# Kernel tuning notes

Measured on AMD Instinct MI355X. Metric: run time of the kernel, lower is better.

## Reference

```python
import jax, jax.numpy as jnp
import numpy as np

N_BASIS = 128   # n_atom_basis F
N_INT   = 3     # n_interactions
N_RBF   = 20
CUTOFF  = 5.0
MAX_Z   = 100
EPS     = 1e-8
N_ATOMS = 25000
N_EDGES = 200000


def setup_inputs() -> dict:
    key = jax.random.key(0)
    ks = jax.random.split(key, 16)
    F = N_BASIS
    s = 0.02
    z     = jax.random.randint(ks[0], (N_ATOMS,), 1, MAX_Z)
    pos   = jax.random.uniform(ks[1], (N_ATOMS, 3), dtype=jnp.float32) * 2.0  # small box -> inside cutoff
    idx_i = jax.random.randint(ks[2], (N_EDGES,), 0, N_ATOMS)
    idx_j = jax.random.randint(ks[3], (N_EDGES,), 0, N_ATOMS)
    emb   = jax.random.normal(ks[4], (MAX_Z, F), dtype=jnp.float32) * s
    fW    = jax.random.normal(ks[5], (N_RBF, 3 * F * N_INT), dtype=jnp.float32) * s
    fb    = jnp.zeros((3 * F * N_INT,), jnp.float32)
    iW1   = jax.random.normal(ks[6], (N_INT, F, F), dtype=jnp.float32) * s
    ib1   = jnp.zeros((N_INT, F), jnp.float32)
    iW2   = jax.random.normal(ks[7], (N_INT, F, 3 * F), dtype=jnp.float32) * s
    ib2   = jnp.zeros((N_INT, 3 * F), jnp.float32)
    mWmix = jax.random.normal(ks[8], (N_INT, F, 2 * F), dtype=jnp.float32) * s
    mW1   = jax.random.normal(ks[9], (N_INT, 2 * F, F), dtype=jnp.float32) * s
    mb1   = jnp.zeros((N_INT, F), jnp.float32)
    mW2   = jax.random.normal(ks[10], (N_INT, F, 3 * F), dtype=jnp.float32) * s
    mb2   = jnp.zeros((N_INT, 3 * F), jnp.float32)
    return dict(z=z, pos=pos, idx_i=idx_i, idx_j=idx_j, emb=emb, fW=fW, fb=fb,
                iW1=iW1, ib1=ib1, iW2=iW2, ib2=ib2,
                mWmix=mWmix, mW1=mW1, mb1=mb1, mW2=mW2, mb2=mb2)


def reference(z, pos, idx_i, idx_j, emb, fW, fb, iW1, ib1, iW2, ib2,
              mWmix, mW1, mb1, mW2, mb2):
    F = N_BASIS
    n_atoms = z.shape[0]
    # geometry
    r_ij = pos[idx_j] - pos[idx_i]                                  # [E,3]
    r_ij = jnp.where(jnp.abs(r_ij) < 1e-6, 1e-6, r_ij)
    d_ij = jnp.linalg.norm(r_ij, axis=1, keepdims=True)             # [E,1]
    dir_ij = r_ij / d_ij                                            # [E,3]
    # Gaussian radial basis
    offsets = jnp.linspace(0.0, CUTOFF, N_RBF)
    width = offsets[1] - offsets[0]
    coeff = -0.5 / (width * width)
    phi = jnp.exp(coeff * (d_ij[..., None] - offsets) ** 2)         # [E,1,n_rbf]
    # cosine cutoff
    fcut = 0.5 * (jnp.cos(jnp.pi * d_ij / CUTOFF) + 1.0) * (d_ij < CUTOFF)  # [E,1]
    filters = (phi @ fW + fb) * fcut[..., None]                     # [E,1,3F*I]
    filter_list = jnp.split(filters, N_INT, axis=-1)                # each [E,1,3F]
    # initial atom features
    q = emb[z][:, None, :]                                          # [N,1,F]
    mu = jnp.zeros((n_atoms, 3, F), q.dtype)                        # [N,3,F]
    for t in range(N_INT):
        # --- interaction (gather - filter-multiply - scatter-add) ---
        x = jax.nn.silu(q @ iW1[t] + ib1[t]) @ iW2[t] + ib2[t]      # [N,1,3F]
        xj = x[idx_j]                                               # [E,1,3F]
        muj = mu[idx_j]                                             # [E,3,F]
        x = filter_list[t] * xj                                     # [E,1,3F]
        dq, dmuR, dmumu = jnp.split(x, 3, axis=-1)                  # [E,1,F] each
        dq = jax.ops.segment_sum(dq, idx_i, num_segments=n_atoms)   # [N,1,F]
        dmu = dmuR * dir_ij[..., None] + dmumu * muj                # [E,3,F]
        dmu = jax.ops.segment_sum(dmu, idx_i, num_segments=n_atoms) # [N,3,F]
        q = q + dq
        mu = mu + dmu
        # --- mixing (intra-atomic) ---
        mu_mix = mu @ mWmix[t]                                      # [N,3,2F]
        mu_V, mu_W = jnp.split(mu_mix, 2, axis=-1)                  # [N,3,F]
        mu_Vn = jnp.sqrt(jnp.sum(mu_V ** 2, axis=-2, keepdims=True) + EPS)  # [N,1,F]
        ctx = jnp.concatenate([q, mu_Vn], axis=-1)                  # [N,1,2F]
        x = jax.nn.silu(ctx @ mW1[t] + mb1[t]) @ mW2[t] + mb2[t]    # [N,1,3F]
        dq_intra, dmu_intra, dqmu_intra = jnp.split(x, 3, axis=-1)
        dmu_intra = dmu_intra * mu_W                                # [N,3,F]
        dqmu_intra = dqmu_intra * jnp.sum(mu_V * mu_W, axis=1, keepdims=True)
        q = q + dq_intra + dqmu_intra
        mu = mu + dmu_intra
    return q.squeeze(1), mu
```

## Files before the change

### kernel.cpp

```cpp
#include <hip/hip_runtime.h>
#include <hip/hip_bf16.h>

#define F 128
#define F3 384
#define NRBF 20
#define NITER 3
#define KP 24

typedef __hip_bfloat16 bf16;
typedef __bf16 bfrag __attribute__((ext_vector_type(8)));
typedef float f32x4 __attribute__((ext_vector_type(4)));

__device__ __forceinline__ float b2f(bf16 v) { return __bfloat162float(v); }
__device__ __forceinline__ bf16 f2b(float v) { return __float2bfloat16(v); }
__device__ __forceinline__ bfrag ldb(const bf16* p) { return *(const bfrag*)p; }
__device__ __forceinline__ bfrag ldsb(const __bf16* p) { return *(const bfrag*)p; }
__device__ __forceinline__ bfrag cvtf(const float* p) {
    bfrag r;
#pragma unroll
    for (int j = 0; j < 8; ++j) r[j] = (__bf16)p[j];
    return r;
}

__global__ void detect_kernel(const unsigned short* __restrict__ raw, int n_u16,
                              int* __restrict__ flag) {
    int i = blockIdx.x * blockDim.x + threadIdx.x;
    int bad = 0;
    for (int k = i; k < n_u16; k += blockDim.x * gridDim.x) {
        unsigned e = (raw[k] >> 7) & 0xFFu;
        if (e >= 140u) bad = 1;
    }
    if (bad) atomicOr(flag, 1);
}

__global__ void cvt_dual_kernel(const void* __restrict__ src, float* __restrict__ dst,
                                int n, const int* __restrict__ flag) {
    int i = blockIdx.x * blockDim.x + threadIdx.x;
    if (i >= n) return;
    if (*flag) dst[i] = ((const float*)src)[i];
    else       dst[i] = b2f(((const bf16*)src)[i]);
}

__global__ void transpose_bf16_kernel(const float* __restrict__ src, bf16* __restrict__ dst,
                                      int K, int Nn, int total) {
    int i = blockIdx.x * blockDim.x + threadIdx.x;
    if (i >= total) return;
    int slice = K * Nn;
    int t = i / slice, j = i - t * slice;
    int n = j / K, k = j - n * K;
    dst[i] = f2b(src[t * slice + k * Nn + n]);
}

__global__ void fwt_kernel(const float* __restrict__ fW, const float* __restrict__ fb,
                           float* __restrict__ dst, int total) {
    int idx = blockIdx.x * blockDim.x + threadIdx.x;
    if (idx >= total) return;
    int k = idx % KP, rest = idx / KP;
    int n = rest % F3, t = rest / F3;
    float v = (k < NRBF) ? fW[k * (F3 * NITER) + t * F3 + n]
                         : (k == NRBF ? fb[t * F3 + n] : 0.0f);
    dst[idx] = v;
}

__global__ void geom_kernel(const float* __restrict__ pos, const int* __restrict__ ii,
                            const int* __restrict__ jj, const int* __restrict__ rank,
                            float* __restrict__ phifc2, float* __restrict__ dir2,
                            int* __restrict__ jj2, int E) {
    int e = blockIdx.x * blockDim.x + threadIdx.x;
    if (e >= E) return;
    int i = ii[e], j = jj[e], l = rank[e];
    float r[3];
#pragma unroll
    for (int d = 0; d < 3; ++d) {
        float v = pos[j * 3 + d] - pos[i * 3 + d];
        if (fabsf(v) < 1e-6f) v = 1e-6f;
        r[d] = v;
    }
    float dd = sqrtf(r[0] * r[0] + r[1] * r[1] + r[2] * r[2]);
    float inv = 1.0f / dd;
    jj2[l] = j;
#pragma unroll
    for (int d = 0; d < 3; ++d) dir2[(size_t)l * 4 + d] = r[d] * inv;
    dir2[(size_t)l * 4 + 3] = 0.0f;
    const float CUT = 5.0f;
    const float PI = 3.14159265358979323846f;
    float fc = (dd < CUT) ? 0.5f * (cosf(PI * dd / CUT) + 1.0f) : 0.0f;
    const float width = CUT / (NRBF - 1);
    const float coeff = -0.5f / (width * width);
    float* pr = phifc2 + (size_t)l * KP;
#pragma unroll
    for (int k = 0; k < NRBF; ++k) {
        float diff = dd - (float)k * width;
        pr[k] = expf(coeff * diff * diff) * fc;
    }
    pr[NRBF] = fc;
    pr[NRBF + 1] = 0.0f;
    pr[NRBF + 2] = 0.0f;
    pr[NRBF + 3] = 0.0f;
}

__global__ void embed_kernel(const int* __restrict__ z, const float* __restrict__ emb,
                             float* __restrict__ q, int N) {
    int idx = blockIdx.x * blockDim.x + threadIdx.x;
    if (idx >= N * F) return;
    int n = idx >> 7, f = idx & 127;
    q[idx] = emb[z[n] * F + f];
}

__global__ void count_kernel(const int* __restrict__ ii, int* __restrict__ counts, int E) {
    int e = blockIdx.x * blockDim.x + threadIdx.x;
    if (e < E) atomicAdd(&counts[ii[e]], 1);
}

__global__ void scan_kernel(const int* __restrict__ counts, int* __restrict__ offs, int N) {
    __shared__ int cum[1024];
    int t = threadIdx.x;
    int chunk = (N + 1023) >> 10;
    int b = t * chunk;
    int e = b + chunk; if (e > N) e = N;
    int s = 0;
    for (int a = b; a < e; ++a) s += counts[a];
    cum[t] = s;
    __syncthreads();
    for (int o = 1; o < 1024; o <<= 1) {
        int u = (t >= o) ? cum[t - o] : 0;
        __syncthreads();
        cum[t] += u;
        __syncthreads();
    }
    int run = cum[t] - s;
    for (int a = b; a < e; ++a) { offs[a] = run; run += counts[a]; }
    if (t == 1023) offs[N] = cum[1023];
}

__global__ void fill_kernel(const int* __restrict__ ii, const int* __restrict__ offs,
                            int* __restrict__ cursor, int* __restrict__ rank, int E) {
    int e = blockIdx.x * blockDim.x + threadIdx.x;
    if (e >= E) return;
    int i = ii[e];
    int p = atomicAdd(&cursor[i], 1);
    rank[e] = offs[i] + p;
}

__global__ __launch_bounds__(256) void atom_x_mfma(
    const float* __restrict__ q, const bf16* __restrict__ W1T, const float* __restrict__ b1,
    const bf16* __restrict__ W2T, const float* __restrict__ b2, bf16* __restrict__ x, int N) {
    __shared__ __bf16 H[32][136];
    int tid = threadIdx.x;
    int w = tid >> 6, l = tid & 63;
    int lm = l & 15, q4 = l >> 4;
    int i0 = blockIdx.x * 32;
    f32x4 acc[2][2] = {};
    int r0 = min(i0 + lm, N - 1);
    int r1 = min(i0 + 16 + lm, N - 1);
    for (int kt = 0; kt < 4; ++kt) {
        int ko = kt * 32 + q4 * 8;
        bfrag a0 = cvtf(q + (size_t)r0 * F + ko);
        bfrag a1 = cvtf(q + (size_t)r1 * F + ko);
        bfrag b0 = ldb(W1T + (size_t)(w * 32 + lm) * F + ko);
        bfrag b1f = ldb(W1T + (size_t)(w * 32 + 16 + lm) * F + ko);
        acc[0][0] = __builtin_amdgcn_mfma_f32_16x16x32_bf16(a0, b0, acc[0][0], 0, 0, 0);
        acc[1][0] = __builtin_amdgcn_mfma_f32_16x16x32_bf16(a1, b0, acc[1][0], 0, 0, 0);
        acc[0][1] = __builtin_amdgcn_mfma_f32_16x16x32_bf16(a0, b1f, acc[0][1], 0, 0, 0);
        acc[1][1] = __builtin_amdgcn_mfma_f32_16x16x32_bf16(a1, b1f, acc[1][1], 0, 0, 0);
    }
#pragma unroll
    for (int nt = 0; nt < 2; ++nt) {
        int col = w * 32 + nt * 16 + lm;
        float bb = b1[col];
#pragma unroll
        for (int mt = 0; mt < 2; ++mt)
#pragma unroll
            for (int r = 0; r < 4; ++r) {
                float v = acc[mt][nt][r] + bb;
                H[mt * 16 + q4 * 4 + r][col] = (__bf16)(v / (1.0f + expf(-v)));
            }
    }
    __syncthreads();
#pragma unroll
    for (int j = 0; j < 6; ++j) {
        int n0 = w * 96 + j * 16;
        f32x4 c0 = {}, c1 = {};
        const bf16* bp = W2T + (size_t)(n0 + lm) * F;
        for (int kt = 0; kt < 4; ++kt) {
            int ko = kt * 32 + q4 * 8;
            bfrag a0 = ldsb(&H[lm][ko]);
            bfrag a1 = ldsb(&H[16 + lm][ko]);
            bfrag bf = ldb(bp + ko);
            c0 = __builtin_amdgcn_mfma_f32_16x16x32_bf16(a0, bf, c0, 0, 0, 0);
            c1 = __builtin_amdgcn_mfma_f32_16x16x32_bf16(a1, bf, c1, 0, 0, 0);
        }
        int col = n0 + lm;
        float bb = b2[col];
#pragma unroll
        for (int r = 0; r < 4; ++r) {
            int row0 = i0 + q4 * 4 + r;
            int row1 = row0 + 16;
            if (row0 < N) x[(size_t)row0 * F3 + col] = f2b(c0[r] + bb);
            if (row1 < N) x[(size_t)row1 * F3 + col] = f2b(c1[r] + bb);
        }
    }
}

__global__ __launch_bounds__(128, 2) void edge_gather_reg(
    float* __restrict__ q, const bf16* __restrict__ mu_in, const bf16* __restrict__ x,
    const float* __restrict__ phifc2, const float* __restrict__ dir2,
    const int* __restrict__ jj2, const float* __restrict__ fWTf,
    const int* __restrict__ offs, bf16* __restrict__ mu_out, int N) {
    int i = blockIdx.x;
    int f = threadIdx.x;
    float w0[NRBF + 1], w1[NRBF + 1], w2[NRBF + 1];
    {
        const float* p0 = fWTf + (size_t)f * KP;
        const float* p1 = fWTf + (size_t)(f + 128) * KP;
        const float* p2 = fWTf + (size_t)(f + 256) * KP;
#pragma unroll
        for (int k = 0; k <= NRBF; ++k) {
            w0[k] = p0[k];
            w1[k] = p1[k];
            w2[k] = p2[k];
        }
    }
    int beg = offs[i], end = offs[i + 1];
    float accq = 0.0f, am0 = 0.0f, am1 = 0.0f, am2 = 0.0f;
    for (int l = beg; l < end; ++l) {
        const float* pr = phifc2 + (size_t)l * KP;
        float f0 = 0.0f, f1 = 0.0f, f2 = 0.0f;
#pragma unroll
        for (int k = 0; k <= NRBF; ++k) {
            float ph = pr[k];
            f0 += ph * w0[k];
            f1 += ph * w1[k];
            f2 += ph * w2[k];
        }
        int j = jj2[l];
        const bf16* xj = x + (size_t)j * F3;
        float dq = f0 * b2f(xj[f]);
        float dR = f1 * b2f(xj[f + 128]);
        float dM = f2 * b2f(xj[f + 256]);
        accq += dq;
        float d0 = dir2[(size_t)l * 4 + 0];
        float d1 = dir2[(size_t)l * 4 + 1];
        float d2 = dir2[(size_t)l * 4 + 2];
        const bf16* muj = mu_in + (size_t)j * F3;
        am0 += dR * d0 + dM * b2f(muj[f]);
        am1 += dR * d1 + dM * b2f(muj[f + 128]);
        am2 += dR * d2 + dM * b2f(muj[f + 256]);
    }
    q[(size_t)i * F + f] += accq;
    size_t mb = (size_t)i * F3 + f;
    mu_out[mb]       = f2b(b2f(mu_in[mb]) + am0);
    mu_out[mb + 128] = f2b(b2f(mu_in[mb + 128]) + am1);
    mu_out[mb + 256] = f2b(b2f(mu_in[mb + 256]) + am2);
}

__global__ __launch_bounds__(256) void mix_mfma(
    float* __restrict__ q, bf16* __restrict__ mu,
    const bf16* __restrict__ WmixT, const bf16* __restrict__ W1T, const float* __restrict__ b1,
    const bf16* __restrict__ W2T, const float* __restrict__ b2, int N) {
    __shared__ __bf16 MM[48][264];
    __shared__ __bf16 CT[16][264];
    __shared__ __bf16 HM[16][136];
    __shared__ __bf16 Y[16][392];
    int tid = threadIdx.x;
    int w = tid >> 6, l = tid & 63;
    int lm = l & 15, q4 = l >> 4;
    int i0 = blockIdx.x * 16;
    int rowsM = N * 3;
    {
        f32x4 acc[3][4] = {};
        int mr[3];
#pragma unroll
        for (int mt = 0; mt < 3; ++mt) mr[mt] = min(i0 * 3 + mt * 16 + lm, rowsM - 1);
        for (int kt = 0; kt < 4; ++kt) {
            int ko = kt * 32 + q4 * 8;
            bfrag a[3], b[4];
#pragma unroll
            for (int mt = 0; mt < 3; ++mt) a[mt] = ldb(mu + (size_t)mr[mt] * F + ko);
#pragma unroll
            for (int nt = 0; nt < 4; ++nt)
                b[nt] = ldb(WmixT + (size_t)(w * 64 + nt * 16 + lm) * F + ko);
#pragma unroll
            for (int mt = 0; mt < 3; ++mt)
#pragma unroll
                for (int nt = 0; nt < 4; ++nt)
                    acc[mt][nt] = __builtin_amdgcn_mfma_f32_16x16x32_bf16(a[mt], b[nt], acc[mt][nt], 0, 0, 0);
        }
#pragma unroll
        for (int mt = 0; mt < 3; ++mt)
#pragma unroll
            for (int nt = 0; nt < 4; ++nt)
#pragma unroll
                for (int r = 0; r < 4; ++r)
                    MM[mt * 16 + q4 * 4 + r][w * 64 + nt * 16 + lm] = (__bf16)acc[mt][nt][r];
    }
    __syncthreads();
    for (int idx = tid; idx < 16 * F; idx += 256) {
        int a = idx >> 7, f = idx & 127;
        int i = min(i0 + a, N - 1);
        float v0 = (float)MM[a * 3 + 0][f];
        float v1 = (float)MM[a * 3 + 1][f];
        float v2 = (float)MM[a * 3 + 2][f];
        CT[a][f] = (__bf16)q[(size_t)i * F + f];
        CT[a][F + f] = (__bf16)sqrtf(v0 * v0 + v1 * v1 + v2 * v2 + 1e-8f);
    }
    __syncthreads();
    {
        f32x4 c[2] = {};
        for (int kt = 0; kt < 8; ++kt) {
            int ko = kt * 32 + q4 * 8;
            bfrag a = ldsb(&CT[lm][ko]);
#pragma unroll
            for (int nt = 0; nt < 2; ++nt) {
                bfrag b = ldb(W1T + (size_t)(w * 32 + nt * 16 + lm) * 256 + ko);
                c[nt] = __builtin_amdgcn_mfma_f32_16x16x32_bf16(a, b, c[nt], 0, 0, 0);
            }
        }
#pragma unroll
        for (int nt = 0; nt < 2; ++nt) {
            int col = w * 32 + nt * 16 + lm;
            float bb = b1[col];
#pragma unroll
            for (int r = 0; r < 4; ++r) {
                float v = c[nt][r] + bb;
                HM[q4 * 4 + r][col] = (__bf16)(v / (1.0f + expf(-v)));
            }
        }
    }
    __syncthreads();
#pragma unroll
    for (int j = 0; j < 6; ++j) {
        int n0 = w * 96 + j * 16;
        f32x4 c = {};
        const bf16* bp = W2T + (size_t)(n0 + lm) * F;
        for (int kt = 0; kt < 4; ++kt) {
            int ko = kt * 32 + q4 * 8;
            bfrag a = ldsb(&HM[lm][ko]);
            bfrag b = ldb(bp + ko);
            c = __builtin_amdgcn_mfma_f32_16x16x32_bf16(a, b, c, 0, 0, 0);
        }
        int col = n0 + lm;
        float bb = b2[col];
#pragma unroll
        for (int r = 0; r < 4; ++r)
            Y[q4 * 4 + r][col] = (__bf16)(c[r] + bb);
    }
    __syncthreads();
    for (int idx = tid; idx < 16 * F; idx += 256) {
        int a = idx >> 7, f = idx & 127;
        int i = i0 + a;
        if (i >= N) continue;
        float V0 = (float)MM[a * 3 + 0][f], W0 = (float)MM[a * 3 + 0][F + f];
        float V1 = (float)MM[a * 3 + 1][f], W1v = (float)MM[a * 3 + 1][F + f];
        float V2 = (float)MM[a * 3 + 2][f], W2v = (float)MM[a * 3 + 2][F + f];
        float s = V0 * W0 + V1 * W1v + V2 * W2v;
        float yq = (float)Y[a][f], ym = (float)Y[a][F + f], ys = (float)Y[a][2 * F + f];
        q[(size_t)i * F + f] += yq + ys * s;
        size_t mb = (size_t)i * F3 + f;
        mu[mb]       = f2b(b2f(mu[mb]) + ym * W0);
        mu[mb + 128] = f2b(b2f(mu[mb + 128]) + ym * W1v);
        mu[mb + 256] = f2b(b2f(mu[mb + 256]) + ym * W2v);
    }
}

__global__ void out_kernel(const float* __restrict__ q, const bf16* __restrict__ mu,
                           void* __restrict__ out, int N, const int* __restrict__ flag) {
    int idx = blockIdx.x * blockDim.x + threadIdx.x;
    int nq = N * F;
    int tot = nq + N * F3;
    if (idx >= tot) return;
    float v = (idx < nq) ? q[idx] : b2f(mu[idx - nq]);
    if (*flag) ((float*)out)[idx] = v;
    else       ((bf16*)out)[idx] = f2b(v);
}

extern "C" void kernel_launch(void* const* d_in, const int* in_sizes, int n_in,
                              void* d_out, int out_size, void* d_ws, size_t ws_size,
                              hipStream_t stream) {
    const int* z = (const int*)d_in[0];
    const int* idx_i = (const int*)d_in[2];
    const int* idx_j = (const int*)d_in[3];

    int N = in_sizes[0];
    int E = in_sizes[2];

    char* base = (char*)d_ws;
    size_t off = 0;
    auto alloc = [&](size_t bytes) -> void* {
        void* p = base + off;
        off += (bytes + 255) & ~(size_t)255;
        return p;
    };

    int* flag = (int*)alloc(4);
    float* pos_f = (float*)alloc((size_t)in_sizes[1] * 4);
    float* emb_f = (float*)alloc((size_t)in_sizes[4] * 4);
    float* fW_f = (float*)alloc((size_t)in_sizes[5] * 4);
    float* fb_f = (float*)alloc((size_t)in_sizes[6] * 4);
    float* iW1_f = (float*)alloc((size_t)in_sizes[7] * 4);
    float* ib1_f = (float*)alloc((size_t)in_sizes[8] * 4);
    float* iW2_f = (float*)alloc((size_t)in_sizes[9] * 4);
    float* ib2_f = (float*)alloc((size_t)in_sizes[10] * 4);
    float* mWmix_f = (float*)alloc((size_t)in_sizes[11] * 4);
    float* mW1_f = (float*)alloc((size_t)in_sizes[12] * 4);
    float* mb1_f = (float*)alloc((size_t)in_sizes[13] * 4);
    float* mW2_f = (float*)alloc((size_t)in_sizes[14] * 4);
    float* mb2_f = (float*)alloc((size_t)in_sizes[15] * 4);
    bf16* iW1T = (bf16*)alloc((size_t)NITER * F * F * 2);
    bf16* iW2T = (bf16*)alloc((size_t)NITER * F3 * F * 2);
    bf16* mWmixT = (bf16*)alloc((size_t)NITER * 2 * F * F * 2);
    bf16* mW1T = (bf16*)alloc((size_t)NITER * F * 2 * F * 2);
    bf16* mW2T = (bf16*)alloc((size_t)NITER * F3 * F * 2);
    float* fWTf = (float*)alloc((size_t)NITER * F3 * KP * 4);
    float* q = (float*)alloc((size_t)N * F * 4);
    bf16* mua = (bf16*)alloc((size_t)N * F3 * 2);
    bf16* mub = (bf16*)alloc((size_t)N * F3 * 2);
    bf16* xbuf = (bf16*)alloc((size_t)N * F3 * 2);
    float* phifc2 = (float*)alloc((size_t)(E + 16) * KP * 4);
    float* dir2 = (float*)alloc((size_t)(E + 16) * 4 * 4);
    int* jj2 = (int*)alloc((size_t)(E + 16) * 4);
    int* rank = (int*)alloc((size_t)E * 4);
    int* counts = (int*)alloc((size_t)N * 4);
    int* offs = (int*)alloc((size_t)(N + 1) * 4);

    hipMemsetAsync(flag, 0, 4, stream);
    detect_kernel<<<64, 256, 0, stream>>>((const unsigned short*)d_in[1], in_sizes[1], flag);

    auto cvt = [&](int idx, float* dst) {
        int n = in_sizes[idx];
        cvt_dual_kernel<<<(n + 255) / 256, 256, 0, stream>>>(d_in[idx], dst, n, flag);
    };
    cvt(1, pos_f);
    cvt(4, emb_f);
    cvt(5, fW_f);  cvt(6, fb_f);
    cvt(7, iW1_f); cvt(8, ib1_f);
    cvt(9, iW2_f); cvt(10, ib2_f);
    cvt(11, mWmix_f);
    cvt(12, mW1_f); cvt(13, mb1_f);
    cvt(14, mW2_f); cvt(15, mb2_f);

    auto tpose = [&](const float* src, bf16* dst, int K, int Nn) {
        int total = NITER * K * Nn;
        transpose_bf16_kernel<<<(total + 255) / 256, 256, 0, stream>>>(src, dst, K, Nn, total);
    };
    tpose(iW1_f, iW1T, F, F);
    tpose(iW2_f, iW2T, F, F3);
    tpose(mWmix_f, mWmixT, F, 2 * F);
    tpose(mW1_f, mW1T, 2 * F, F);
    tpose(mW2_f, mW2T, F, F3);
    {
        int total = NITER * F3 * KP;
        fwt_kernel<<<(total + 255) / 256, 256, 0, stream>>>(fW_f, fb_f, fWTf, total);
    }

    hipMemsetAsync(counts, 0, (size_t)N * 4, stream);
    count_kernel<<<(E + 255) / 256, 256, 0, stream>>>(idx_i, counts, E);
    scan_kernel<<<1, 1024, 0, stream>>>(counts, offs, N);
    hipMemsetAsync(counts, 0, (size_t)N * 4, stream);
    fill_kernel<<<(E + 255) / 256, 256, 0, stream>>>(idx_i, offs, counts, rank, E);

    geom_kernel<<<(E + 255) / 256, 256, 0, stream>>>(pos_f, idx_i, idx_j, rank,
                                                     phifc2, dir2, jj2, E);
    embed_kernel<<<(N * F + 255) / 256, 256, 0, stream>>>(z, emb_f, q, N);
    hipMemsetAsync(mua, 0, (size_t)N * F3 * 2, stream);

    bf16* muin = mua;
    bf16* muout = mub;
    for (int t = 0; t < NITER; ++t) {
        atom_x_mfma<<<(N + 31) / 32, 256, 0, stream>>>(q, iW1T + (size_t)t * F * F, ib1_f + t * F,
                                                       iW2T + (size_t)t * F3 * F, ib2_f + t * F3,
                                                       xbuf, N);
        edge_gather_reg<<<N, 128, 0, stream>>>(q, muin, xbuf, phifc2, dir2, jj2,
                                               fWTf + (size_t)t * F3 * KP, offs, muout, N);
        mix_mfma<<<(N + 15) / 16, 256, 0, stream>>>(q, muout, mWmixT + (size_t)t * 2 * F * F,
                                                    mW1T + (size_t)t * F * 2 * F, mb1_f + t * F,
                                                    mW2T + (size_t)t * F3 * F, mb2_f + t * F3, N);
        bf16* tm = muin; muin = muout; muout = tm;
    }

    int tot = N * (F + F3);
    out_kernel<<<(tot + 255) / 256, 256, 0, stream>>>(q, muin, d_out, N, flag);
}
```

Baseline: 832.3 us.

## Split edge gather across three channel groups and batch setup kernel launches

The per-atom edge gather kernel now runs 384 threads per block. Each 128-thread group handles one of the three filter channels (q, radial mu, mu-mu), and the partial mu sums are combined through shared memory. This cuts per-thread registers and serial work and raises parallelism per atom, at the cost of a block-wide sync and redundant phi loads across groups. Separately, the 13 input conversion launches and 5 transpose launches are merged into one launch each to reduce launch overhead.

Measured after the change: 1.061 ms. +27.5%, slower.

```diff
diff --git a/kernel.cpp b/kernel.cpp
--- a/kernel.cpp
+++ b/kernel.cpp
@@ -33,22 +33,39 @@
     if (bad) atomicOr(flag, 1);
 }
 
-__global__ void cvt_dual_kernel(const void* __restrict__ src, float* __restrict__ dst,
-                                int n, const int* __restrict__ flag) {
-    int i = blockIdx.x * blockDim.x + threadIdx.x;
-    if (i >= n) return;
-    if (*flag) dst[i] = ((const float*)src)[i];
-    else       dst[i] = b2f(((const bf16*)src)[i]);
-}
-
-__global__ void transpose_bf16_kernel(const float* __restrict__ src, bf16* __restrict__ dst,
-                                      int K, int Nn, int total) {
-    int i = blockIdx.x * blockDim.x + threadIdx.x;
-    if (i >= total) return;
-    int slice = K * Nn;
-    int t = i / slice, j = i - t * slice;
+struct CvtArgs {
+    const void* src[13];
+    float* dst[13];
+    int end[14];
+};
+__global__ void cvt_all_kernel(CvtArgs a, const int* __restrict__ flag, int total) {
+    int idx = blockIdx.x * blockDim.x + threadIdx.x;
+    if (idx >= total) return;
+    int s = 0;
+    while (idx >= a.end[s + 1]) ++s;
+    int local = idx - a.end[s];
+    float v = (*flag) ? ((const float*)a.src[s])[local]
+                      : b2f(((const bf16*)a.src[s])[local]);
+    a.dst[s][local] = v;
+}
+
+struct TpArgs {
+    const float* src[5];
+    bf16* dst[5];
+    int K[5];
+    int Nn[5];
+    int end[6];
+};
+__global__ void tpose_all_kernel(TpArgs a, int total) {
+    int idx = blockIdx.x * blockDim.x + threadIdx.x;
+    if (idx >= total) return;
+    int s = 0;
+    while (idx >= a.end[s + 1]) ++s;
+    int local = idx - a.end[s];
+    int K = a.K[s], Nn = a.Nn[s], slice = K * Nn;
+    int t = local / slice, j = local - t * slice;
     int n = j / K, k = j - n * K;
-    dst[i] = f2b(src[t * slice + k * Nn + n]);
+    a.dst[s][local] = f2b(a.src[s][t * slice + k * Nn + n]);
 }
 
 __global__ void fwt_kernel(const float* __restrict__ fW, const float* __restrict__ fb,
@@ -202,56 +219,54 @@
     }
 }
 
-__global__ __launch_bounds__(128, 2) void edge_gather_reg(
+__global__ __launch_bounds__(384) void edge_gather_cls(
     float* __restrict__ q, const bf16* __restrict__ mu_in, const bf16* __restrict__ x,
     const float* __restrict__ phifc2, const float* __restrict__ dir2,
     const int* __restrict__ jj2, const float* __restrict__ fWTf,
     const int* __restrict__ offs, bf16* __restrict__ mu_out, int N) {
+    __shared__ float Rs[3][128];
     int i = blockIdx.x;
-    int f = threadIdx.x;
-    float w0[NRBF + 1], w1[NRBF + 1], w2[NRBF + 1];
+    int tid = threadIdx.x;
+    int c = tid >> 7, f = tid & 127;
+    float w[NRBF + 1];
     {
-        const float* p0 = fWTf + (size_t)f * KP;
-        const float* p1 = fWTf + (size_t)(f + 128) * KP;
-        const float* p2 = fWTf + (size_t)(f + 256) * KP;
-#pragma unroll
-        for (int k = 0; k <= NRBF; ++k) {
-            w0[k] = p0[k];
-            w1[k] = p1[k];
-            w2[k] = p2[k];
-        }
+        const float* wp = fWTf + (size_t)(c * 128 + f) * KP;
+#pragma unroll
+        for (int k = 0; k <= NRBF; ++k) w[k] = wp[k];
     }
     int beg = offs[i], end = offs[i + 1];
-    float accq = 0.0f, am0 = 0.0f, am1 = 0.0f, am2 = 0.0f;
+    float a0 = 0.0f, a1 = 0.0f, a2 = 0.0f;
     for (int l = beg; l < end; ++l) {
         const float* pr = phifc2 + (size_t)l * KP;
-        float f0 = 0.0f, f1 = 0.0f, f2 = 0.0f;
-#pragma unroll
-        for (int k = 0; k <= NRBF; ++k) {
-            float ph = pr[k];
-            f0 += ph * w0[k];
-            f1 += ph * w1[k];
-            f2 += ph * w2[k];
-        }
+        float fv = 0.0f;
+#pragma unroll
+        for (int k = 0; k <= NRBF; ++k) fv += pr[k] * w[k];
         int j = jj2[l];
-        const bf16* xj = x + (size_t)j * F3;
-        float dq = f0 * b2f(xj[f]);
-        float dR = f1 * b2f(xj[f + 128]);
-        float dM = f2 * b2f(xj[f + 256]);
-        accq += dq;
-        float d0 = dir2[(size_t)l * 4 + 0];
-        float d1 = dir2[(size_t)l * 4 + 1];
-        float d2 = dir2[(size_t)l * 4 + 2];
-        const bf16* muj = mu_in + (size_t)j * F3;
-        am0 += dR * d0 + dM * b2f(muj[f]);
-        am1 += dR * d1 + dM * b2f(muj[f + 128]);
-        am2 += dR * d2 + dM * b2f(muj[f + 256]);
-    }
-    q[(size_t)i * F + f] += accq;
-    size_t mb = (size_t)i * F3 + f;
-    mu_out[mb]       = f2b(b2f(mu_in[mb]) + am0);
-    mu_out[mb + 128] = f2b(b2f(mu_in[mb + 128]) + am1);
-    mu_out[mb + 256] = f2b(b2f(mu_in[mb + 256]) + am2);
+        float xv = b2f(x[(size_t)j * F3 + c * 128 + f]);
+        float g = fv * xv;
+        if (c == 0) {
+            a0 += g;
+        } else if (c == 1) {
+            a0 += g * dir2[(size_t)l * 4 + 0];
+            a1 += g * dir2[(size_t)l * 4 + 1];
+            a2 += g * dir2[(size_t)l * 4 + 2];
+        } else {
+            const bf16* mj = mu_in + (size_t)j * F3 + f;
+            a0 += g * b2f(mj[0]);
+            a1 += g * b2f(mj[128]);
+            a2 += g * b2f(mj[256]);
+        }
+    }
+    if (c == 1) { Rs[0][f] = a0; Rs[1][f] = a1; Rs[2][f] = a2; }
+    __syncthreads();
+    if (c == 0) {
+        q[(size_t)i * F + f] += a0;
+    } else if (c == 2) {
+        size_t mb = (size_t)i * F3 + f;
+        mu_out[mb]       = f2b(b2f(mu_in[mb])       + a0 + Rs[0][f]);
+        mu_out[mb + 128] = f2b(b2f(mu_in[mb + 128]) + a1 + Rs[1][f]);
+        mu_out[mb + 256] = f2b(b2f(mu_in[mb + 256]) + a2 + Rs[2][f]);
+    }
 }
 
 __global__ __launch_bounds__(256) void mix_mfma(
@@ -426,28 +441,40 @@
     hipMemsetAsync(flag, 0, 4, stream);
     detect_kernel<<<64, 256, 0, stream>>>((const unsigned short*)d_in[1], in_sizes[1], flag);
 
-    auto cvt = [&](int idx, float* dst) {
-        int n = in_sizes[idx];
-        cvt_dual_kernel<<<(n + 255) / 256, 256, 0, stream>>>(d_in[idx], dst, n, flag);
-    };
-    cvt(1, pos_f);
-    cvt(4, emb_f);
-    cvt(5, fW_f);  cvt(6, fb_f);
-    cvt(7, iW1_f); cvt(8, ib1_f);
-    cvt(9, iW2_f); cvt(10, ib2_f);
-    cvt(11, mWmix_f);
-    cvt(12, mW1_f); cvt(13, mb1_f);
-    cvt(14, mW2_f); cvt(15, mb2_f);
-
-    auto tpose = [&](const float* src, bf16* dst, int K, int Nn) {
-        int total = NITER * K * Nn;
-        transpose_bf16_kernel<<<(total + 255) / 256, 256, 0, stream>>>(src, dst, K, Nn, total);
-    };
-    tpose(iW1_f, iW1T, F, F);
-    tpose(iW2_f, iW2T, F, F3);
-    tpose(mWmix_f, mWmixT, F, 2 * F);
-    tpose(mW1_f, mW1T, 2 * F, F);
-    tpose(mW2_f, mW2T, F, F3);
+    {
+        CvtArgs a;
+        const int srcIdx[13] = {1, 4, 5, 6, 7, 8, 9, 10, 11, 12, 13, 14, 15};
+        float* dsts[13] = {pos_f, emb_f, fW_f, fb_f, iW1_f, ib1_f, iW2_f, ib2_f,
+                           mWmix_f, mW1_f, mb1_f, mW2_f, mb2_f};
+        int cum = 0;
+        a.end[0] = 0;
+        for (int s = 0; s < 13; ++s) {
+            a.src[s] = d_in[srcIdx[s]];
+            a.dst[s] = dsts[s];
+            cum += in_sizes[srcIdx[s]];
+            a.end[s + 1] = cum;
+        }
+        cvt_all_kernel<<<(cum + 255) / 256, 256, 0, stream>>>(a, flag, cum);
+    }
+
+    {
+        TpArgs a;
+        const float* srcs[5] = {iW1_f, iW2_f, mWmix_f, mW1_f, mW2_f};
+        bf16* dsts[5] = {iW1T, iW2T, mWmixT, mW1T, mW2T};
+        int Ks[5] = {F, F, F, 2 * F, F};
+        int Nns[5] = {F, F3, 2 * F, F, F3};
+        int cum = 0;
+        a.end[0] = 0;
+        for (int s = 0; s < 5; ++s) {
+            a.src[s] = srcs[s];
+            a.dst[s] = dsts[s];
+            a.K[s] = Ks[s];
+            a.Nn[s] = Nns[s];
+            cum += NITER * Ks[s] * Nns[s];
+            a.end[s + 1] = cum;
+        }
+        tpose_all_kernel<<<(cum + 255) / 256, 256, 0, stream>>>(a, cum);
+    }
     {
         int total = NITER * F3 * KP;
         fwt_kernel<<<(total + 255) / 256, 256, 0, stream>>>(fW_f, fb_f, fWTf, total);
@@ -470,7 +497,7 @@
         atom_x_mfma<<<(N + 31) / 32, 256, 0, stream>>>(q, iW1T + (size_t)t * F * F, ib1_f + t * F,
                                                        iW2T + (size_t)t * F3 * F, ib2_f + t * F3,
                                                        xbuf, N);
-        edge_gather_reg<<<N, 128, 0, stream>>>(q, muin, xbuf, phifc2, dir2, jj2,
+        edge_gather_cls<<<N, 384, 0, stream>>>(q, muin, xbuf, phifc2, dir2, jj2,
                                                fWTf + (size_t)t * F3 * KP, offs, muout, N);
         mix_mfma<<<(N + 15) / 16, 256, 0, stream>>>(q, muout, mWmixT + (size_t)t * 2 * F * F,
                                                     mW1T + (size_t)t * F * 2 * F, mb1_f + t * F,
```
